# Kernel optimization log

Measured on AMD Instinct MI355X. Metric: run time of the kernel, lower is better.

Reference implementation:

```python
import jax, jax.numpy as jnp
import numpy as np

B, T, D = 2, 128, 1024
H, R, Dk, Dv = 8, 8, 64, 64


def setup_inputs() -> dict:
    key = jax.random.key(0)
    ks = jax.random.split(key, 11)
    w = lambda k, shp: jax.random.normal(k, shp, dtype=jnp.float32) * 0.02
    return {
        "hidden_states": jax.random.normal(ks[0], (B, T, D), dtype=jnp.float32),
        "Wq": w(ks[1], (D, H * Dk)),
        "Wk": w(ks[2], (D, H * Dk)),
        "Wv": w(ks[3], (D, H * Dv)),
        "Wb": w(ks[4], (D, H * R)),
        "Wtg": w(ks[5], (D, H * R)),
        "mode_logits": jax.random.normal(ks[6], (H, R), dtype=jnp.float32) * 0.1,
        "log_decay": jax.random.normal(ks[7], (H, R), dtype=jnp.float32) * 0.1,
        "omega_log_scale": jax.random.normal(ks[8], (H, R), dtype=jnp.float32) * 0.1,
        "Wg": w(ks[9], (D, H * Dv)),
        "Wo": w(ks[10], (H * Dv, D)),
    }


def _forward(x, Wq, Wk, Wv, Wb, Wtg, mode_logits, log_decay, omega_log_scale, Wg, Wo):
    b, t, _ = x.shape
    # projections
    q = (x @ Wq).reshape(b, t, H, Dk)
    k = (x @ Wk).reshape(b, t, H, Dk)
    v = (x @ Wv).reshape(b, t, H, Dv)
    beta = jax.nn.sigmoid((x @ Wb).reshape(b, t, H, R))
    tg = jax.nn.sigmoid((x @ Wtg).reshape(b, t, H, R))
    # spectral mode parameters
    pair_idx = jnp.arange(0, Dk, 2, dtype=jnp.float32)
    inv_freq = 1.0 / (10000.0 ** (pair_idx / Dk))            # [Dk/2]
    omega = jnp.exp(omega_log_scale)[..., None] * inv_freq    # [H,R,Dk/2]
    omega_full = jnp.repeat(omega, 2, axis=-1)                # [H,R,Dk] (repeat_interleave)
    cos_w = jnp.cos(omega_full)[None, :, :, None, :]          # [1,H,R,1,Dk]
    sin_w = jnp.sin(omega_full)[None, :, :, None, :]
    rho = jnp.exp(-jax.nn.softplus(log_decay))                # [H,R]
    mode_w = jax.nn.softmax(mode_logits, axis=-1)             # [H,R]

    # time-major for scan
    qT = jnp.moveaxis(q, 1, 0)
    kT = jnp.moveaxis(k, 1, 0)
    vT = jnp.moveaxis(v, 1, 0)
    betaT = jnp.moveaxis(beta, 1, 0)
    tgT = jnp.moveaxis(tg, 1, 0)

    def step(carry, xs):
        sr, si = carry                      # [B,H,R,Dv,Dk] each
        q_t, k_t, v_t, b_t, g_t = xs
        decay = (g_t * rho)[..., None, None]            # [B,H,R,1,1]
        rot_r = decay * (cos_w * sr - sin_w * si)
        rot_i = decay * (sin_w * sr + cos_w * si)
        pred = jnp.einsum('bhrvk,bhk->bhrv', rot_r, k_t)
        err = v_t[:, :, None, :] - pred                  # [B,H,R,Dv]
        write = err[..., None] * k_t[:, :, None, None, :]
        sr_new = rot_r + b_t[..., None, None] * write
        read = jnp.einsum('bhrvk,bhk->bhrv', sr_new, q_t)
        y = jnp.einsum('bhrv,hr->bhv', read, mode_w)     # [B,H,Dv]
        return (sr_new, rot_i), y

    s0 = jnp.zeros((b, H, R, Dv, Dk), dtype=x.dtype)
    _, ys = jax.lax.scan(step, (s0, s0), (qT, kT, vT, betaT, tgT))
    o = jnp.moveaxis(ys, 0, 1)                           # [B,T,H,Dv]
    gate = jax.nn.sigmoid((x @ Wg).reshape(b, t, H, Dv))
    o = (o * gate).reshape(b, t, H * Dv)
    return o @ Wo


def reference(hidden_states, Wq, Wk, Wv, Wb, Wtg, mode_logits, log_decay,
              omega_log_scale, Wg, Wo):
    return _forward(hidden_states, Wq, Wk, Wv, Wb, Wtg, mode_logits,
                    log_decay, omega_log_scale, Wg, Wo)
```

## Files before the change

### kernel.cpp

```cpp
#include <hip/hip_runtime.h>
#include <math.h>

#define T_ 128
#define NPROJ 2176
#define CH 32

typedef __attribute__((ext_vector_type(8))) short short8;
typedef __attribute__((ext_vector_type(4))) float float4v;
typedef __attribute__((ext_vector_type(2))) float float2v;

__device__ __forceinline__ ushort f2bf(float x) {
    unsigned u = __float_as_uint(x);
    u += 0x7FFF + ((u >> 16) & 1);
    return (ushort)(u >> 16);
}
__device__ __forceinline__ unsigned pack_bf(float a, float b) {
    unsigned ua = (__float_as_uint(a) + 0x8000u) >> 16;
    unsigned ub = (__float_as_uint(b) + 0x8000u) & 0xffff0000u;
    return ua | ub;
}
__device__ __forceinline__ float bf_lo(unsigned w) { return __uint_as_float(w << 16); }
__device__ __forceinline__ float bf_hi(unsigned w) { return __uint_as_float(w & 0xffff0000u); }

template<int CTRL>
__device__ __forceinline__ float dpp_add(float x) {
    int xi = __float_as_int(x);
    int yi = __builtin_amdgcn_update_dpp(xi, xi, CTRL, 0xF, 0xF, false);
    return x + __int_as_float(yi);
}

__global__ __launch_bounds__(256) void prep_kernel(
    const float* __restrict__ x,
    const float* __restrict__ Wq, const float* __restrict__ Wk,
    const float* __restrict__ Wv, const float* __restrict__ Wb,
    const float* __restrict__ Wtg, const float* __restrict__ Wg,
    const float* __restrict__ Wo,
    const float* __restrict__ mode_logits, const float* __restrict__ log_decay,
    const float* __restrict__ ols,
    float* __restrict__ cosw, float* __restrict__ sinw,
    float* __restrict__ rho, float* __restrict__ modew,
    ushort* __restrict__ xb, ushort* __restrict__ wtb, ushort* __restrict__ wotb,
    float* __restrict__ Acomb)
{
    __shared__ ushort tile[64][68];
    const int blk = blockIdx.x, tid = threadIdx.x;
    if (blk < 16) {
        int idx = blk * 256 + tid;
        if (idx >= 64 * 64) return;
        int t = idx >> 6;
        int k = idx & 63;
        int h = t >> 3;
        if (k == 0) {
            float ld = log_decay[t];
            rho[t] = 1.0f / (1.0f + expf(ld));
            float m = -1e30f;
            for (int i = 0; i < 8; i++) m = fmaxf(m, mode_logits[h * 8 + i]);
            float sum = 0.0f;
            for (int i = 0; i < 8; i++) sum += expf(mode_logits[h * 8 + i] - m);
            modew[t] = expf(mode_logits[t] - m) / sum;
        }
        float osc = expf(ols[t]);
        int p = k >> 1;
        float invf = expf(-((float)(2 * p) / 64.0f) * logf(10000.0f));
        float w = osc * invf;
        cosw[idx] = cosf(w);
        sinw[idx] = sinf(w);
        return;
    }
    if (blk < 80) {
        int base = (blk - 16) * 4096 + tid * 16;
        float4 f0 = *(const float4*)&x[base];
        float4 f1 = *(const float4*)&x[base + 4];
        float4 f2 = *(const float4*)&x[base + 8];
        float4 f3 = *(const float4*)&x[base + 12];
        short8 o0, o1;
        o0[0]=f2bf(f0.x); o0[1]=f2bf(f0.y); o0[2]=f2bf(f0.z); o0[3]=f2bf(f0.w);
        o0[4]=f2bf(f1.x); o0[5]=f2bf(f1.y); o0[6]=f2bf(f1.z); o0[7]=f2bf(f1.w);
        o1[0]=f2bf(f2.x); o1[1]=f2bf(f2.y); o1[2]=f2bf(f2.z); o1[3]=f2bf(f2.w);
        o1[4]=f2bf(f3.x); o1[5]=f2bf(f3.y); o1[6]=f2bf(f3.z); o1[7]=f2bf(f3.w);
        *(short8*)&xb[base] = o0;
        *(short8*)&xb[base + 8] = o1;
        return;
    }
    if (blk >= 752) {
        int base = (blk - 752) * 4096 + tid * 16;
        float4 z = make_float4(0.f, 0.f, 0.f, 0.f);
        *(float4*)&Acomb[base] = z;
        *(float4*)&Acomb[base + 4] = z;
        *(float4*)&Acomb[base + 8] = z;
        *(float4*)&Acomb[base + 12] = z;
        return;
    }
    const float* src; int ld, c0, n0, k0, ldd; ushort* dst;
    if (blk < 624) {
        int b3 = blk - 80; int nt = b3 >> 4, kt = b3 & 15;
        n0 = nt * 64; k0 = kt * 64;
        if (n0 < 512)       { src = Wq;  c0 = n0;        ld = 512; }
        else if (n0 < 1024) { src = Wk;  c0 = n0 - 512;  ld = 512; }
        else if (n0 < 1536) { src = Wv;  c0 = n0 - 1024; ld = 512; }
        else if (n0 < 1600) { src = Wb;  c0 = n0 - 1536; ld = 64;  }
        else if (n0 < 1664) { src = Wtg; c0 = n0 - 1600; ld = 64;  }
        else                { src = Wg;  c0 = n0 - 1664; ld = 512; }
        dst = wtb; ldd = 1024;
    } else {
        int b4 = blk - 624; int nt = b4 >> 3, kt = b4 & 7;
        n0 = nt * 64; k0 = kt * 64;
        src = Wo; c0 = n0; ld = 1024; dst = wotb; ldd = 512;
    }
    #pragma unroll
    for (int rep = 0; rep < 4; rep++) {
        int k = rep * 16 + (tid >> 4);
        int nc = (tid & 15) * 4;
        float4 f = *(const float4*)&src[(size_t)(k0 + k) * ld + c0 + nc];
        tile[nc + 0][k] = f2bf(f.x);
        tile[nc + 1][k] = f2bf(f.y);
        tile[nc + 2][k] = f2bf(f.z);
        tile[nc + 3][k] = f2bf(f.w);
    }
    __syncthreads();
    #pragma unroll
    for (int rep = 0; rep < 4; rep++) {
        int n = rep * 16 + (tid >> 4);
        int kc = (tid & 15) * 4;
        uint2 uu = *(const uint2*)&tile[n][kc];
        *(uint2*)&dst[(size_t)(n0 + n) * ldd + k0 + kc] = uu;
    }
}

__global__ __launch_bounds__(256, 2) void proj_mfma(const ushort* __restrict__ Ab,
        const ushort* __restrict__ BTb, float* __restrict__ proj)
{
    __shared__ ushort sA[2][64][40];
    __shared__ ushort sB[2][64][40];
    const int n0 = blockIdx.x * 64, m0 = blockIdx.y * 64;
    const int tid = threadIdx.x;
    const int lane = tid & 63, w = tid >> 6;
    const int wm = w & 1, wn = w >> 1;
    const int l16 = lane & 15, quad = lane >> 4;
    const int srow = tid >> 2, skq = (tid & 3) * 8;
    const ushort* Ag = Ab + (size_t)(m0 + srow) * 1024 + skq;
    const ushort* Bg = BTb + (size_t)(n0 + srow) * 1024 + skq;
    short8 ra = *(const short8*)Ag;
    short8 rb = *(const short8*)Bg;
    float4v acc00 = {0,0,0,0}, acc01 = {0,0,0,0}, acc10 = {0,0,0,0}, acc11 = {0,0,0,0};
    for (int kt = 0; kt < 32; kt++) {
        const int cb = kt & 1;
        *(short8*)&sA[cb][srow][skq] = ra;
        *(short8*)&sB[cb][srow][skq] = rb;
        __syncthreads();
        if (kt + 1 < 32) {
            ra = *(const short8*)(Ag + (kt + 1) * 32);
            rb = *(const short8*)(Bg + (kt + 1) * 32);
        }
        short8 a0 = *(const short8*)&sA[cb][wm * 32 + l16][quad * 8];
        short8 a1 = *(const short8*)&sA[cb][wm * 32 + 16 + l16][quad * 8];
        short8 b0 = *(const short8*)&sB[cb][wn * 32 + l16][quad * 8];
        short8 b1 = *(const short8*)&sB[cb][wn * 32 + 16 + l16][quad * 8];
        acc00 = __builtin_amdgcn_mfma_f32_16x16x32_bf16(a0, b0, acc00, 0, 0, 0);
        acc01 = __builtin_amdgcn_mfma_f32_16x16x32_bf16(a0, b1, acc01, 0, 0, 0);
        acc10 = __builtin_amdgcn_mfma_f32_16x16x32_bf16(a1, b0, acc10, 0, 0, 0);
        acc11 = __builtin_amdgcn_mfma_f32_16x16x32_bf16(a1, b1, acc11, 0, 0, 0);
    }
    const bool sig = (n0 >= 1536);
    const int colb = n0 + wn * 32 + l16;
    const int rowb = m0 + wm * 32 + quad * 4;
    #pragma unroll
    for (int r2 = 0; r2 < 4; r2++) {
        float v00 = acc00[r2], v01 = acc01[r2], v10 = acc10[r2], v11 = acc11[r2];
        if (sig) {
            v00 = 1.0f / (1.0f + expf(-v00));
            v01 = 1.0f / (1.0f + expf(-v01));
            v10 = 1.0f / (1.0f + expf(-v10));
            v11 = 1.0f / (1.0f + expf(-v11));
        }
        proj[(size_t)(rowb + r2) * NPROJ + colb] = v00;
        proj[(size_t)(rowb + r2) * NPROJ + colb + 16] = v01;
        proj[(size_t)(rowb + 16 + r2) * NPROJ + colb] = v10;
        proj[(size_t)(rowb + 16 + r2) * NPROJ + colb + 16] = v11;
    }
}

__global__ __launch_bounds__(256, 2) void scan_kernel(const float* __restrict__ proj,
        const float* __restrict__ cosw, const float* __restrict__ sinw,
        const float* __restrict__ rho, const float* __restrict__ modew,
        float* __restrict__ Acomb)
{
    __shared__ uint2 qks[2][CH][16][2];
    __shared__ float2 vg[2][CH][16];
    __shared__ float sc4[2][CH][4];
    __shared__ float obuf[CH][16];

    const int bi = blockIdx.x;
    const int s  = bi & 3;
    const int hr = (bi >> 2) & 63;
    const int b  = bi >> 8;
    const int h = hr >> 3, r = hr & 7;
    const int tid = threadIdx.x;
    const int vl = tid >> 4;
    const int kl = tid & 15;

    float2v cw0, cw1, sw0, sw1;
    cw0.x = cosw[hr * 64 + kl * 4 + 0]; cw0.y = cosw[hr * 64 + kl * 4 + 1];
    cw1.x = cosw[hr * 64 + kl * 4 + 2]; cw1.y = cosw[hr * 64 + kl * 4 + 3];
    sw0.x = sinw[hr * 64 + kl * 4 + 0]; sw0.y = sinw[hr * 64 + kl * 4 + 1];
    sw1.x = sinw[hr * 64 + kl * 4 + 2]; sw1.y = sinw[hr * 64 + kl * 4 + 3];
    const float rho_hr = rho[hr];
    const float mw = modew[hr];
    float2v sr0 = {0,0}, sr1 = {0,0}, si0 = {0,0}, si1 = {0,0};

    const float* pb = proj + (size_t)b * T_ * NPROJ;
    const int qbase = h * 64;
    const int kbase = 512 + h * 64;
    const int vbase = 1024 + h * 64 + s * 16;
    const int gbase = 1664 + h * 64 + s * 16;
    const int boff  = 1536 + h * 8 + r;
    const int goff  = 1600 + h * 8 + r;

    {
        #pragma unroll
        for (int rep = 0; rep < 4; rep++) {
            int idx = rep * 256 + tid;
            int t = idx >> 5, sub = idx & 31;
            const float* row = pb + (size_t)t * NPROJ;
            float4 f = *(const float4*)(row + (sub < 16 ? qbase + sub * 4
                                                        : kbase + (sub - 16) * 4));
            uint2 pk2; pk2.x = pack_bf(f.x, f.y); pk2.y = pack_bf(f.z, f.w);
            qks[0][t][sub & 15][sub < 16 ? 1 : 0] = pk2;
        }
        #pragma unroll
        for (int rep = 0; rep < 2; rep++) {
            int idx = rep * 256 + tid;
            int t = idx >> 4, v2 = idx & 15;
            const float* row = pb + (size_t)t * NPROJ;
            vg[0][t][v2] = make_float2(row[vbase + v2], row[gbase + v2]);
        }
        if (tid < CH)            sc4[0][tid][0]      = pb[(size_t)tid * NPROJ + boff];
        else if (tid < 2 * CH)   sc4[0][tid - CH][1] = pb[(size_t)(tid - CH) * NPROJ + goff];
    }
    __syncthreads();

    float* dstb = Acomb + ((size_t)b * 128) * 512 + h * 64 + s * 16;

    for (int c = 0; c < T_ / CH; c++) {
        const int cb = c & 1, nb = cb ^ 1;
        const bool have = (c + 1 < T_ / CH);

        float4 g_qk[4]; float2 g_vg[2]; float g_sc = 0.0f;
        if (have) {
            const int t0 = (c + 1) * CH;
            #pragma unroll
            for (int rep = 0; rep < 4; rep++) {
                int idx = rep * 256 + tid;
                int t = idx >> 5, sub = idx & 31;
                const float* row = pb + (size_t)(t0 + t) * NPROJ;
                g_qk[rep] = *(const float4*)(row + (sub < 16 ? qbase + sub * 4
                                                             : kbase + (sub - 16) * 4));
            }
            #pragma unroll
            for (int rep = 0; rep < 2; rep++) {
                int idx = rep * 256 + tid;
                int t = idx >> 4, v2 = idx & 15;
                const float* row = pb + (size_t)(t0 + t) * NPROJ;
                g_vg[rep] = make_float2(row[vbase + v2], row[gbase + v2]);
            }
            if (tid < CH)          g_sc = pb[(size_t)(t0 + tid) * NPROJ + boff];
            else if (tid < 2 * CH) g_sc = pb[(size_t)(t0 + tid - CH) * NPROJ + goff];
        }

        {
            int t = tid >> 3, j = tid & 7;
            uint4 wa = *(const uint4*)&qks[cb][t][2 * j][0];
            uint4 wb = *(const uint4*)&qks[cb][t][2 * j + 1][0];
            float p = bf_lo(wa.x) * bf_lo(wa.z) + bf_hi(wa.x) * bf_hi(wa.z)
                    + bf_lo(wa.y) * bf_lo(wa.w) + bf_hi(wa.y) * bf_hi(wa.w)
                    + bf_lo(wb.x) * bf_lo(wb.z) + bf_hi(wb.x) * bf_hi(wb.z)
                    + bf_lo(wb.y) * bf_lo(wb.w) + bf_hi(wb.y) * bf_hi(wb.w);
            p = dpp_add<0xB1>(p);
            p = dpp_add<0x4E>(p);
            p = dpp_add<0x141>(p);
            if (j == 0) sc4[cb][t][2] = p;
        }
        if (c > 0) {
            #pragma unroll
            for (int rep = 0; rep < 2; rep++) {
                int idx = rep * 256 + tid;
                int t = idx >> 4, v2 = idx & 15;
                atomicAdd(dstb + (size_t)((c - 1) * CH + t) * 512 + v2, obuf[t][v2]);
            }
        }
        __syncthreads();

        const float2* vgb = &vg[cb][0][0];
        const float4* svb = (const float4*)&sc4[cb][0][0];

        uint4 w = *(const uint4*)&qks[cb][0][kl][0];
        float4 sv = svb[0];
        float2 vgv = vgb[vl];
        #pragma unroll
        for (int t = 0; t < CH; t++) {
            uint4 w_n; float4 sv_n; float2 vg_n;
            if (t + 1 < CH) {
                w_n = *(const uint4*)&qks[cb][t + 1][kl][0];
                sv_n = svb[t + 1];
                vg_n = vgb[(t + 1) * 16 + vl];
            }

            float2v k0; k0.x = bf_lo(w.x); k0.y = bf_hi(w.x);
            float2v k1; k1.x = bf_lo(w.y); k1.y = bf_hi(w.y);
            float2v q0; q0.x = bf_lo(w.z); q0.y = bf_hi(w.z);
            float2v q1; q1.x = bf_lo(w.w); q1.y = bf_hi(w.w);

            const float decay = sv.y * rho_hr;
            float2v t1 = cw0 * sr0 - sw0 * si0;
            float2v u1 = sw0 * sr0 + cw0 * si0;
            float2v t2 = cw1 * sr1 - sw1 * si1;
            float2v u2 = sw1 * sr1 + cw1 * si1;
            float2v d2; d2.x = decay; d2.y = decay;
            float2v rr0 = d2 * t1, rr1 = d2 * t2;
            si0 = d2 * u1; si1 = d2 * u2;

            float2v pk2 = rr0 * k0 + rr1 * k1;
            float2v pq2 = rr0 * q0 + rr1 * q1;
            float pk = pk2.x + pk2.y;
            float pq = pq2.x + pq2.y;
            pk = dpp_add<0xB1>(pk);  pq = dpp_add<0xB1>(pq);
            pk = dpp_add<0x4E>(pk);  pq = dpp_add<0x4E>(pq);
            pk = dpp_add<0x141>(pk); pq = dpp_add<0x141>(pq);
            pk = dpp_add<0x140>(pk); pq = dpp_add<0x140>(pq);

            const float sc = sv.x * (vgv.x - pk);
            float2v sc2; sc2.x = sc; sc2.y = sc;
            sr0 = rr0 + sc2 * k0;
            sr1 = rr1 + sc2 * k1;
            const float rp = pq + sc * sv.z;
            if (kl == 0) obuf[t][vl] = mw * rp * vgv.y;

            w = w_n; sv = sv_n; vgv = vg_n;
        }

        if (have) {
            #pragma unroll
            for (int rep = 0; rep < 4; rep++) {
                int idx = rep * 256 + tid;
                int t = idx >> 5, sub = idx & 31;
                float4 f = g_qk[rep];
                uint2 pk2; pk2.x = pack_bf(f.x, f.y); pk2.y = pack_bf(f.z, f.w);
                qks[nb][t][sub & 15][sub < 16 ? 1 : 0] = pk2;
            }
            #pragma unroll
            for (int rep = 0; rep < 2; rep++) {
                int idx = rep * 256 + tid;
                int t = idx >> 4, v2 = idx & 15;
                vg[nb][t][v2] = g_vg[rep];
            }
            if (tid < CH)          sc4[nb][tid][0]      = g_sc;
            else if (tid < 2 * CH) sc4[nb][tid - CH][1] = g_sc;
        }
        __syncthreads();
    }
    #pragma unroll
    for (int rep = 0; rep < 2; rep++) {
        int idx = rep * 256 + tid;
        int t = idx >> 4, v2 = idx & 15;
        atomicAdd(dstb + (size_t)(3 * CH + t) * 512 + v2, obuf[t][v2]);
    }
}

__global__ __launch_bounds__(256, 2) void out_mfma(const float* __restrict__ Af,
        const ushort* __restrict__ BTb, float* __restrict__ C)
{
    __shared__ ushort sA[2][64][40];
    __shared__ ushort sB[2][64][40];
    const int n0 = blockIdx.x * 64, m0 = blockIdx.y * 64;
    const int tid = threadIdx.x;
    const int lane = tid & 63, w = tid >> 6;
    const int wm = w & 1, wn = w >> 1;
    const int l16 = lane & 15, quad = lane >> 4;
    const int srow = tid >> 2, skq = (tid & 3) * 8;
    const float* Ag = Af + (size_t)(m0 + srow) * 512 + skq;
    const ushort* Bg = BTb + (size_t)(n0 + srow) * 512 + skq;
    float4 fa0 = *(const float4*)Ag;
    float4 fa1 = *(const float4*)(Ag + 4);
    short8 rb = *(const short8*)Bg;
    float4v acc00 = {0,0,0,0}, acc01 = {0,0,0,0}, acc10 = {0,0,0,0}, acc11 = {0,0,0,0};
    for (int kt = 0; kt < 16; kt++) {
        const int cb = kt & 1;
        short8 ra;
        ra[0]=f2bf(fa0.x); ra[1]=f2bf(fa0.y); ra[2]=f2bf(fa0.z); ra[3]=f2bf(fa0.w);
        ra[4]=f2bf(fa1.x); ra[5]=f2bf(fa1.y); ra[6]=f2bf(fa1.z); ra[7]=f2bf(fa1.w);
        *(short8*)&sA[cb][srow][skq] = ra;
        *(short8*)&sB[cb][srow][skq] = rb;
        __syncthreads();
        if (kt + 1 < 16) {
            fa0 = *(const float4*)(Ag + (kt + 1) * 32);
            fa1 = *(const float4*)(Ag + (kt + 1) * 32 + 4);
            rb = *(const short8*)(Bg + (kt + 1) * 32);
        }
        short8 a0 = *(const short8*)&sA[cb][wm * 32 + l16][quad * 8];
        short8 a1 = *(const short8*)&sA[cb][wm * 32 + 16 + l16][quad * 8];
        short8 b0 = *(const short8*)&sB[cb][wn * 32 + l16][quad * 8];
        short8 b1 = *(const short8*)&sB[cb][wn * 32 + 16 + l16][quad * 8];
        acc00 = __builtin_amdgcn_mfma_f32_16x16x32_bf16(a0, b0, acc00, 0, 0, 0);
        acc01 = __builtin_amdgcn_mfma_f32_16x16x32_bf16(a0, b1, acc01, 0, 0, 0);
        acc10 = __builtin_amdgcn_mfma_f32_16x16x32_bf16(a1, b0, acc10, 0, 0, 0);
        acc11 = __builtin_amdgcn_mfma_f32_16x16x32_bf16(a1, b1, acc11, 0, 0, 0);
    }
    const int colb = n0 + wn * 32 + l16;
    const int rowb = m0 + wm * 32 + quad * 4;
    #pragma unroll
    for (int r2 = 0; r2 < 4; r2++) {
        C[(size_t)(rowb + r2) * 1024 + colb] = acc00[r2];
        C[(size_t)(rowb + r2) * 1024 + colb + 16] = acc01[r2];
        C[(size_t)(rowb + 16 + r2) * 1024 + colb] = acc10[r2];
        C[(size_t)(rowb + 16 + r2) * 1024 + colb + 16] = acc11[r2];
    }
}

extern "C" void kernel_launch(void* const* d_in, const int* in_sizes, int n_in,
                              void* d_out, int out_size, void* d_ws, size_t ws_size,
                              hipStream_t stream) {
    const float* x   = (const float*)d_in[0];
    const float* Wq  = (const float*)d_in[1];
    const float* Wk  = (const float*)d_in[2];
    const float* Wv  = (const float*)d_in[3];
    const float* Wb  = (const float*)d_in[4];
    const float* Wtg = (const float*)d_in[5];
    const float* ml  = (const float*)d_in[6];
    const float* ldc = (const float*)d_in[7];
    const float* ols = (const float*)d_in[8];
    const float* Wg  = (const float*)d_in[9];
    const float* Wo  = (const float*)d_in[10];
    float* out = (float*)d_out;

    float* ws = (float*)d_ws;
    float* proj    = ws;
    float* cosw    = proj + 256 * NPROJ;
    float* sinw    = cosw + 4096;
    float* rho     = sinw + 4096;
    float* modew   = rho + 64;
    ushort* xb     = (ushort*)(modew + 64);
    ushort* wotb   = (ushort*)((float*)xb + 131072);
    float*  Acomb  = (float*)wotb + 262144;
    ushort* wtb    = (ushort*)(Acomb + 131072);

    prep_kernel<<<784, 256, 0, stream>>>(x, Wq, Wk, Wv, Wb, Wtg, Wg, Wo,
                                         ml, ldc, ols, cosw, sinw, rho, modew,
                                         xb, wtb, wotb, Acomb);
    proj_mfma<<<dim3(34, 4), 256, 0, stream>>>(xb, wtb, proj);
    scan_kernel<<<512, 256, 0, stream>>>(proj, cosw, sinw, rho, modew, Acomb);
    out_mfma<<<dim3(16, 4), 256, 0, stream>>>(Acomb, wotb, out);
}
```

Baseline: 137.3 us.

## Break scan dependency chain via two-step lookahead recurrence with precomputed scalar coefficients

Restructures the per-timestep scan so the cross-lane reductions of state against the next step's k and q are computed one step ahead, using a double-angle rotation (cos2w, sin2w) and per-timestep scalar corrections precomputed in the chunk prologue (k·q, decay-weighted cross terms). The error term at step t then becomes a scalar combination, which takes the DPP reduction off the serial critical path between state updates. Decay is pre-multiplied by rho when staged into shared memory. This adds extra per-step FMAs, more registers, extra prologue reductions and more shared memory, and changes floating-point association.

Result: slower. 143.6 us (+4.5%).

```diff
diff --git a/kernel.cpp b/kernel.cpp
--- a/kernel.cpp
+++ b/kernel.cpp
@@ -187,8 +187,9 @@
 {
     __shared__ uint2 qks[2][CH][16][2];
     __shared__ float2 vg[2][CH][16];
-    __shared__ float sc4[2][CH][4];
+    __shared__ float sc8[2][CH][8];
     __shared__ float obuf[CH][16];
+    __shared__ float cwS[64];
 
     const int bi = blockIdx.x;
     const int s  = bi & 3;
@@ -204,9 +205,14 @@
     cw1.x = cosw[hr * 64 + kl * 4 + 2]; cw1.y = cosw[hr * 64 + kl * 4 + 3];
     sw0.x = sinw[hr * 64 + kl * 4 + 0]; sw0.y = sinw[hr * 64 + kl * 4 + 1];
     sw1.x = sinw[hr * 64 + kl * 4 + 2]; sw1.y = sinw[hr * 64 + kl * 4 + 3];
+    float2v c2w0 = cw0 * cw0 - sw0 * sw0;
+    float2v c2w1 = cw1 * cw1 - sw1 * sw1;
+    float2v s2w0 = cw0 * sw0; s2w0 = s2w0 + s2w0;
+    float2v s2w1 = cw1 * sw1; s2w1 = s2w1 + s2w1;
+
     const float rho_hr = rho[hr];
     const float mw = modew[hr];
-    float2v sr0 = {0,0}, sr1 = {0,0}, si0 = {0,0}, si1 = {0,0};
+    float2v crS0 = {0,0}, crS1 = {0,0}, ciS0 = {0,0}, ciS1 = {0,0};
 
     const float* pb = proj + (size_t)b * T_ * NPROJ;
     const int qbase = h * 64;
@@ -215,6 +221,8 @@
     const int gbase = 1664 + h * 64 + s * 16;
     const int boff  = 1536 + h * 8 + r;
     const int goff  = 1600 + h * 8 + r;
+
+    if (tid < 64) cwS[tid] = cosw[hr * 64 + tid];
 
     {
         #pragma unroll
@@ -234,8 +242,8 @@
             const float* row = pb + (size_t)t * NPROJ;
             vg[0][t][v2] = make_float2(row[vbase + v2], row[gbase + v2]);
         }
-        if (tid < CH)            sc4[0][tid][0]      = pb[(size_t)tid * NPROJ + boff];
-        else if (tid < 2 * CH)   sc4[0][tid - CH][1] = pb[(size_t)(tid - CH) * NPROJ + goff];
+        if (tid < CH)            sc8[0][tid][0]      = pb[(size_t)tid * NPROJ + boff];
+        else if (tid < 2 * CH)   sc8[0][tid - CH][1] = pb[(size_t)(tid - CH) * NPROJ + goff] * rho_hr;
     }
     __syncthreads();
 
@@ -269,16 +277,45 @@
 
         {
             int t = tid >> 3, j = tid & 7;
-            uint4 wa = *(const uint4*)&qks[cb][t][2 * j][0];
-            uint4 wb = *(const uint4*)&qks[cb][t][2 * j + 1][0];
-            float p = bf_lo(wa.x) * bf_lo(wa.z) + bf_hi(wa.x) * bf_hi(wa.z)
-                    + bf_lo(wa.y) * bf_lo(wa.w) + bf_hi(wa.y) * bf_hi(wa.w)
-                    + bf_lo(wb.x) * bf_lo(wb.z) + bf_hi(wb.x) * bf_hi(wb.z)
-                    + bf_lo(wb.y) * bf_lo(wb.w) + bf_hi(wb.y) * bf_hi(wb.w);
-            p = dpp_add<0xB1>(p);
-            p = dpp_add<0x4E>(p);
-            p = dpp_add<0x141>(p);
-            if (j == 0) sc4[cb][t][2] = p;
+            int tp = (t > 0) ? t - 1 : 0;
+            uint4 wl = *(const uint4*)&qks[cb][t][2 * j][0];
+            uint4 wh = *(const uint4*)&qks[cb][t][2 * j + 1][0];
+            uint4 pl = *(const uint4*)&qks[cb][tp][2 * j][0];
+            uint4 ph = *(const uint4*)&qks[cb][tp][2 * j + 1][0];
+            float4 cwa = *(const float4*)&cwS[8 * j];
+            float4 cwb = *(const float4*)&cwS[8 * j + 4];
+            float2v kt0; kt0.x=bf_lo(wl.x); kt0.y=bf_hi(wl.x);
+            float2v kt1; kt1.x=bf_lo(wl.y); kt1.y=bf_hi(wl.y);
+            float2v kt2; kt2.x=bf_lo(wh.x); kt2.y=bf_hi(wh.x);
+            float2v kt3; kt3.x=bf_lo(wh.y); kt3.y=bf_hi(wh.y);
+            float2v qt0; qt0.x=bf_lo(wl.z); qt0.y=bf_hi(wl.z);
+            float2v qt1; qt1.x=bf_lo(wl.w); qt1.y=bf_hi(wl.w);
+            float2v qt2; qt2.x=bf_lo(wh.z); qt2.y=bf_hi(wh.z);
+            float2v qt3; qt3.x=bf_lo(wh.w); qt3.y=bf_hi(wh.w);
+            float2v kp0; kp0.x=bf_lo(pl.x); kp0.y=bf_hi(pl.x);
+            float2v kp1; kp1.x=bf_lo(pl.y); kp1.y=bf_hi(pl.y);
+            float2v kp2; kp2.x=bf_lo(ph.x); kp2.y=bf_hi(ph.x);
+            float2v kp3; kp3.x=bf_lo(ph.y); kp3.y=bf_hi(ph.y);
+            float2v cva; cva.x=cwa.x; cva.y=cwa.y;
+            float2v cvb; cvb.x=cwa.z; cvb.y=cwa.w;
+            float2v cvc; cvc.x=cwb.x; cvc.y=cwb.y;
+            float2v cvd; cvd.x=cwb.z; cvd.y=cwb.w;
+            float2v kqv = kt0*qt0 + kt1*qt1 + kt2*qt2 + kt3*qt3;
+            float2v ck0 = cva*kp0, ck1 = cvb*kp1, ck2 = cvc*kp2, ck3 = cvd*kp3;
+            float2v Bv = ck0*kt0 + ck1*kt1 + ck2*kt2 + ck3*kt3;
+            float2v Fv = ck0*qt0 + ck1*qt1 + ck2*qt2 + ck3*qt3;
+            float kq = kqv.x + kqv.y, Bs = Bv.x + Bv.y, Fs = Fv.x + Fv.y;
+            kq = dpp_add<0xB1>(kq);  Bs = dpp_add<0xB1>(Bs);  Fs = dpp_add<0xB1>(Fs);
+            kq = dpp_add<0x4E>(kq);  Bs = dpp_add<0x4E>(Bs);  Fs = dpp_add<0x4E>(Fs);
+            kq = dpp_add<0x141>(kq); Bs = dpp_add<0x141>(Bs); Fs = dpp_add<0x141>(Fs);
+            if (j == 0) {
+                float dt = sc8[cb][t][1];
+                float dp = (t > 0) ? sc8[cb][t - 1][1] : 0.0f;
+                sc8[cb][t][2] = kq;
+                sc8[cb][t][3] = dt * Bs;
+                sc8[cb][t][4] = dt * Fs;
+                sc8[cb][t][5] = dt * dp;
+            }
         }
         if (c > 0) {
             #pragma unroll
@@ -290,52 +327,106 @@
         }
         __syncthreads();
 
-        const float2* vgb = &vg[cb][0][0];
-        const float4* svb = (const float4*)&sc4[cb][0][0];
-
-        uint4 w = *(const uint4*)&qks[cb][0][kl][0];
-        float4 sv = svb[0];
-        float2 vgv = vgb[vl];
+        float4 svA = *(const float4*)&sc8[cb][0][0];
+        float2 svB = *(const float2*)&sc8[cb][0][4];
+        float2 vgv = vg[cb][0][vl];
+        uint4 w0 = *(const uint4*)&qks[cb][0][kl][0];
+        uint4 wC = *(const uint4*)&qks[cb][1][kl][0];
+        float2v k0a; k0a.x=bf_lo(w0.x); k0a.y=bf_hi(w0.x);
+        float2v k0b; k0b.x=bf_lo(w0.y); k0b.y=bf_hi(w0.y);
+        float2v q0a; q0a.x=bf_lo(w0.z); q0a.y=bf_hi(w0.z);
+        float2v q0b; q0b.x=bf_lo(w0.w); q0b.y=bf_hi(w0.w);
+        float2v kCa; kCa.x=bf_lo(wC.x); kCa.y=bf_hi(wC.x);
+        float2v kCb; kCb.x=bf_lo(wC.y); kCb.y=bf_hi(wC.y);
+        float2v qCa; qCa.x=bf_lo(wC.z); qCa.y=bf_hi(wC.z);
+        float2v qCb; qCb.x=bf_lo(wC.w); qCb.y=bf_hi(wC.w);
+        float d0 = svA.y;
+        float2v dv0; dv0.x = d0; dv0.y = d0;
+        float2v rrPa = dv0 * (cw0 * crS0 - sw0 * ciS0);
+        float2v rrPb = dv0 * (cw1 * crS1 - sw1 * ciS1);
+        float2v ciPa = dv0 * (sw0 * crS0 + cw0 * ciS0);
+        float2v ciPb = dv0 * (sw1 * crS1 + cw1 * ciS1);
+        float2v pkv = rrPa * k0a + rrPb * k0b;
+        float2v pqv = rrPa * q0a + rrPb * q0b;
+        float pk0 = pkv.x + pkv.y, pq0 = pqv.x + pqv.y;
+        float2v r2a = c2w0 * crS0 - s2w0 * ciS0;
+        float2v r2b = c2w1 * crS1 - s2w1 * ciS1;
+        float2v av = r2a * kCa + r2b * kCb;
+        float2v cv = r2a * qCa + r2b * qCb;
+        float A = av.x + av.y, Cc = cv.x + cv.y;
+        pk0 = dpp_add<0xB1>(pk0);  pq0 = dpp_add<0xB1>(pq0);
+        A   = dpp_add<0xB1>(A);    Cc  = dpp_add<0xB1>(Cc);
+        pk0 = dpp_add<0x4E>(pk0);  pq0 = dpp_add<0x4E>(pq0);
+        A   = dpp_add<0x4E>(A);    Cc  = dpp_add<0x4E>(Cc);
+        pk0 = dpp_add<0x141>(pk0); pq0 = dpp_add<0x141>(pq0);
+        A   = dpp_add<0x141>(A);   Cc  = dpp_add<0x141>(Cc);
+        pk0 = dpp_add<0x140>(pk0); pq0 = dpp_add<0x140>(pq0);
+        A   = dpp_add<0x140>(A);   Cc  = dpp_add<0x140>(Cc);
+        float scp = svA.x * (vgv.x - pk0);
+        float rp0 = pq0 + scp * svA.z;
+        if (kl == 0) obuf[0][vl] = mw * rp0 * vgv.y;
+        float2v kPa = k0a, kPb = k0b;
+        svA = *(const float4*)&sc8[cb][1][0];
+        svB = *(const float2*)&sc8[cb][1][4];
+        vgv = vg[cb][1][vl];
+        uint4 wA = *(const uint4*)&qks[cb][2][kl][0];
+
         #pragma unroll
-        for (int t = 0; t < CH; t++) {
-            uint4 w_n; float4 sv_n; float2 vg_n;
+        for (int t = 1; t < CH; t++) {
+            float4 svA_n; float2 svB_n; float2 vg_n; uint4 wB_;
             if (t + 1 < CH) {
-                w_n = *(const uint4*)&qks[cb][t + 1][kl][0];
-                sv_n = svb[t + 1];
-                vg_n = vgb[(t + 1) * 16 + vl];
-            }
-
-            float2v k0; k0.x = bf_lo(w.x); k0.y = bf_hi(w.x);
-            float2v k1; k1.x = bf_lo(w.y); k1.y = bf_hi(w.y);
-            float2v q0; q0.x = bf_lo(w.z); q0.y = bf_hi(w.z);
-            float2v q1; q1.x = bf_lo(w.w); q1.y = bf_hi(w.w);
-
-            const float decay = sv.y * rho_hr;
-            float2v t1 = cw0 * sr0 - sw0 * si0;
-            float2v u1 = sw0 * sr0 + cw0 * si0;
-            float2v t2 = cw1 * sr1 - sw1 * si1;
-            float2v u2 = sw1 * sr1 + cw1 * si1;
-            float2v d2; d2.x = decay; d2.y = decay;
-            float2v rr0 = d2 * t1, rr1 = d2 * t2;
-            si0 = d2 * u1; si1 = d2 * u2;
-
-            float2v pk2 = rr0 * k0 + rr1 * k1;
-            float2v pq2 = rr0 * q0 + rr1 * q1;
-            float pk = pk2.x + pk2.y;
-            float pq = pq2.x + pq2.y;
-            pk = dpp_add<0xB1>(pk);  pq = dpp_add<0xB1>(pq);
-            pk = dpp_add<0x4E>(pk);  pq = dpp_add<0x4E>(pq);
-            pk = dpp_add<0x141>(pk); pq = dpp_add<0x141>(pq);
-            pk = dpp_add<0x140>(pk); pq = dpp_add<0x140>(pq);
-
-            const float sc = sv.x * (vgv.x - pk);
-            float2v sc2; sc2.x = sc; sc2.y = sc;
-            sr0 = rr0 + sc2 * k0;
-            sr1 = rr1 + sc2 * k1;
-            const float rp = pq + sc * sv.z;
+                svA_n = *(const float4*)&sc8[cb][t + 1][0];
+                svB_n = *(const float2*)&sc8[cb][t + 1][4];
+                vg_n  = vg[cb][t + 1][vl];
+            }
+            if (t + 2 < CH) wB_ = *(const uint4*)&qks[cb][t + 2][kl][0];
+
+            float pk = svB.y * A + scp * svA.w;
+            float sc = svA.x * (vgv.x - pk);
+            float rp = svB.y * Cc + scp * svB.x + sc * svA.z;
             if (kl == 0) obuf[t][vl] = mw * rp * vgv.y;
 
-            w = w_n; sv = sv_n; vgv = vg_n;
+            float2v scp2; scp2.x = scp; scp2.y = scp;
+            float2v crPa = rrPa + scp2 * kPa;
+            float2v crPb = rrPb + scp2 * kPb;
+
+            float2v kNa, kNb;
+            float An = 0.0f, Cn = 0.0f;
+            if (t + 1 < CH) {
+                float2v ra2 = c2w0 * crPa - s2w0 * ciPa;
+                float2v rb2 = c2w1 * crPb - s2w1 * ciPb;
+                kNa.x = bf_lo(wA.x); kNa.y = bf_hi(wA.x);
+                kNb.x = bf_lo(wA.y); kNb.y = bf_hi(wA.y);
+                float2v qNa; qNa.x = bf_lo(wA.z); qNa.y = bf_hi(wA.z);
+                float2v qNb; qNb.x = bf_lo(wA.w); qNb.y = bf_hi(wA.w);
+                float2v av2 = ra2 * kNa + rb2 * kNb;
+                float2v cv2 = ra2 * qNa + rb2 * qNb;
+                An = av2.x + av2.y; Cn = cv2.x + cv2.y;
+                An = dpp_add<0xB1>(An);  Cn = dpp_add<0xB1>(Cn);
+                An = dpp_add<0x4E>(An);  Cn = dpp_add<0x4E>(Cn);
+                An = dpp_add<0x141>(An); Cn = dpp_add<0x141>(Cn);
+                An = dpp_add<0x140>(An); Cn = dpp_add<0x140>(Cn);
+            }
+
+            float d = svA.y;
+            float2v dv; dv.x = d; dv.y = d;
+            float2v rrNa = dv * (cw0 * crPa - sw0 * ciPa);
+            float2v rrNb = dv * (cw1 * crPb - sw1 * ciPb);
+            float2v ciNa = dv * (sw0 * crPa + cw0 * ciPa);
+            float2v ciNb = dv * (sw1 * crPb + cw1 * ciPb);
+            rrPa = rrNa; rrPb = rrNb; ciPa = ciNa; ciPb = ciNb;
+            kPa = kCa; kPb = kCb;
+            if (t + 1 < CH) {
+                kCa = kNa; kCb = kNb;
+                A = An; Cc = Cn;
+                svA = svA_n; svB = svB_n; vgv = vg_n; wA = wB_;
+            }
+            scp = sc;
+        }
+        {
+            float2v scp2; scp2.x = scp; scp2.y = scp;
+            crS0 = rrPa + scp2 * kPa; crS1 = rrPb + scp2 * kPb;
+            ciS0 = ciPa; ciS1 = ciPb;
         }
 
         if (have) {
@@ -353,8 +444,8 @@
                 int t = idx >> 4, v2 = idx & 15;
                 vg[nb][t][v2] = g_vg[rep];
             }
-            if (tid < CH)          sc4[nb][tid][0]      = g_sc;
-            else if (tid < 2 * CH) sc4[nb][tid - CH][1] = g_sc;
+            if (tid < CH)          sc8[nb][tid][0]      = g_sc;
+            else if (tid < 2 * CH) sc8[nb][tid - CH][1] = g_sc * rho_hr;
         }
         __syncthreads();
     }
```
